# Kernel optimization log

Measured on AMD Instinct MI355X. Metric: run time of the kernel, lower is better.

The kernel has to match this reference:

```python
import jax, jax.numpy as jnp
import numpy as np


def _maxpool2(x):
    # 2x2 max pool, stride 2, valid padding (H, W even). x: [B,H,W,C]
    B, H, W, C = x.shape
    return x.reshape(B, H // 2, 2, W // 2, 2, C).max(axis=(2, 4))


def setup_inputs() -> dict:
    key = jax.random.key(0)
    ks = jax.random.split(key, 9)
    B, H, W, C = 8, 64, 64, 512
    cfg, ch = C // 8, C // 2
    std = 0.02
    return {
        "x": jax.random.normal(ks[0], (B, H, W, C), jnp.float32),
        "theta_w": jax.random.normal(ks[1], (C, cfg), jnp.float32) * std,
        "theta_b": jnp.zeros((cfg,), jnp.float32),
        "phi_w": jax.random.normal(ks[2], (C, cfg), jnp.float32) * std,
        "phi_b": jnp.zeros((cfg,), jnp.float32),
        "g_w": jax.random.normal(ks[3], (C, ch), jnp.float32) * std,
        "g_b": jnp.zeros((ch,), jnp.float32),
        "o3_w": jax.random.normal(ks[4], (ch, C), jnp.float32) * std,
        "o3_b": jnp.zeros((C,), jnp.float32),
        # original initializes gamma to 0; use 0.1 so the attention branch contributes
        "gamma": jnp.full((1,), 0.1, jnp.float32),
    }


def reference(x, theta_w, theta_b, phi_w, phi_b, g_w, g_b, o3_w, o3_b, gamma):
    B, H, W, C = x.shape
    cfg = theta_w.shape[1]
    ch = g_w.shape[1]
    hw = H * W
    hwd = (H // 2) * (W // 2)

    theta = jnp.einsum("bhwc,cf->bhwf", x, theta_w) + theta_b          # [B,H,W,cfg]
    phi = _maxpool2(jnp.einsum("bhwc,cf->bhwf", x, phi_w) + phi_b)     # [B,H/2,W/2,cfg]
    g = _maxpool2(jnp.einsum("bhwc,cg->bhwg", x, g_w) + g_b)           # [B,H/2,W/2,ch]

    theta_f = theta.reshape(B, hw, cfg)
    phi_f = phi.reshape(B, hwd, cfg)
    g_f = g.reshape(B, hwd, ch)

    # s[b,i,j] = phi[b,i] . theta[b,j]; softmax over j (last axis, Keras default)
    s = jnp.einsum("bif,bjf->bij", phi_f, theta_f)                     # [B,hwd,hw]
    beta = jax.nn.softmax(s, axis=-1)
    # o = matmul(beta, g, transpose_a=True): o[b,j,c] = sum_i beta[b,i,j] g[b,i,c]
    o = jnp.einsum("bij,bic->bjc", beta, g_f)                          # [B,hw,ch]
    o = o.reshape(B, H, W, ch)
    o = jnp.einsum("bhwg,gc->bhwc", o, o3_w) + o3_b                    # [B,H,W,C]
    return gamma * o + x
```

## Files before the change

kernel.cpp:

```cpp
#include <hip/hip_runtime.h>
#include <cstdint>

typedef short short8 __attribute__((ext_vector_type(8)));
typedef float floatx4 __attribute__((ext_vector_type(4)));

__device__ __forceinline__ unsigned short f2bf(float f) {
    unsigned int u = __builtin_bit_cast(unsigned int, f);
    u += 0x7FFFu + ((u >> 16) & 1u);
    return (unsigned short)(u >> 16);
}
__device__ __forceinline__ float bf2f(unsigned short h) {
    unsigned int u = ((unsigned int)h) << 16;
    return __builtin_bit_cast(float, u);
}

__device__ __forceinline__ void async_copy16(const void* g, void* lds) {
    __builtin_amdgcn_global_load_lds(
        (const __attribute__((address_space(1))) void*)g,
        (__attribute__((address_space(3))) void*)lds, 16, 0, 0);
}

__device__ __forceinline__ int swz(int row, int koff) {
    return koff ^ (((row >> 2) & 3) << 4);
}

template<bool AFP32, int EPI>
__global__ __launch_bounds__(256) void mfma_gemm(
    const void* __restrict__ Avoid, const unsigned short* __restrict__ B,
    void* __restrict__ Cout, const float* __restrict__ bias,
    const float* __restrict__ gamma, const float* __restrict__ resid,
    int lda, int ldb, int ldc, int K)
{
    __shared__ unsigned short As[4096];
    __shared__ unsigned short Bs[4096];

    const int tid = threadIdx.x;
    const int wv = tid >> 6, ln = tid & 63;
    const int r16 = ln & 15, q8 = ln >> 4;
    const int wm = (wv >> 1) * 64, wn = (wv & 1) * 64;
    const int m0 = blockIdx.y * 128, n0 = blockIdx.x * 128;

    floatx4 acc[4][4] = {};

    for (int k0 = 0; k0 < K; k0 += 32) {
        if (AFP32) {
            const float* Af = (const float*)Avoid;
            #pragma unroll
            for (int p = 0; p < 4; ++p) {
                int u = p * 256 + tid;
                int row = u >> 3, c4 = u & 7;
                float4 v = *(const float4*)(Af + (size_t)(m0 + row) * lda + k0 + c4 * 4);
                ushort4 h;
                h.x = f2bf(v.x); h.y = f2bf(v.y); h.z = f2bf(v.z); h.w = f2bf(v.w);
                *(ushort4*)&As[row * 32 + c4 * 4] = h;
            }
            #pragma unroll
            for (int q = 0; q < 2; ++q) {
                int chunk = wv * 2 + q;
                int e = (chunk << 9) + ln * 8;
                int row = e >> 5, col = e & 31;
                async_copy16(B + (size_t)(n0 + row) * ldb + (k0 + col), &Bs[chunk << 9]);
            }
        } else {
            const unsigned short* Ag = (const unsigned short*)Avoid;
            #pragma unroll
            for (int q = 0; q < 2; ++q) {
                int chunk = wv * 2 + q;
                int e = (chunk << 9) + ln * 8;
                int row = e >> 5, col = e & 31;
                async_copy16(Ag + (size_t)(m0 + row) * lda + (k0 + col), &As[chunk << 9]);
                async_copy16(B + (size_t)(n0 + row) * ldb + (k0 + col), &Bs[chunk << 9]);
            }
        }
        __syncthreads();

        short8 af[4], bff[4];
        #pragma unroll
        for (int i = 0; i < 4; ++i) {
            af[i]  = *(const short8*)&As[(wm + i * 16 + r16) * 32 + q8 * 8];
            bff[i] = *(const short8*)&Bs[(wn + i * 16 + r16) * 32 + q8 * 8];
        }
        #pragma unroll
        for (int mi = 0; mi < 4; ++mi)
            #pragma unroll
            for (int ni = 0; ni < 4; ++ni)
                acc[mi][ni] = __builtin_amdgcn_mfma_f32_16x16x32_bf16(
                    af[mi], bff[ni], acc[mi][ni], 0, 0, 0);
        __syncthreads();
    }

    if (EPI == 2) {
        float* C = (float*)Cout;
        const float gm = gamma[0];
        #pragma unroll
        for (int ni = 0; ni < 4; ++ni) {
            const int n = n0 + wn + ni * 16 + r16;
            const float bs = bias[n];
            #pragma unroll
            for (int mi = 0; mi < 4; ++mi)
                #pragma unroll
                for (int r = 0; r < 4; ++r) {
                    int m = m0 + wm + mi * 16 + q8 * 4 + r;
                    C[(size_t)m * ldc + n] = gm * (acc[mi][ni][r] + bs) + resid[(size_t)m * ldc + n];
                }
        }
    } else {
        unsigned short* C = (unsigned short*)Cout;
        #pragma unroll
        for (int ni = 0; ni < 4; ++ni) {
            const int n = n0 + wn + ni * 16 + r16;
            const float bs = bias[n];
            #pragma unroll
            for (int mi = 0; mi < 4; ++mi)
                #pragma unroll
                for (int r = 0; r < 4; ++r) {
                    int m = m0 + wm + mi * 16 + q8 * 4 + r;
                    C[(size_t)m * ldc + n] = f2bf(acc[mi][ni][r] + bs);
                }
        }
    }
}

__global__ __launch_bounds__(256) void phase1_l_kernel(
    const unsigned short* __restrict__ tpgF,
    const unsigned short* __restrict__ phiP,
    float* __restrict__ lbuf)
{
    __shared__ unsigned short th_s[8192];
    __shared__ unsigned short ph_s[4096];
    const int tid = threadIdx.x, wv = tid >> 6, ln = tid & 63;
    const int r16 = ln & 15, q8 = ln >> 4, lsub = ln >> 3, l8 = ln & 7;
    const int jsp = blockIdx.x, i0 = blockIdx.y * 64, b = blockIdx.z;

    #pragma unroll
    for (int q = 0; q < 2; ++q) {
        int chunk = wv * 2 + q, row = chunk * 8 + lsub;
        int so = swz(row, l8 * 8);
        async_copy16(phiP + (size_t)(b * 1024 + i0 + row) * 64 + so, &ph_s[chunk * 512]);
    }

    float colsum[4] = {0.f, 0.f, 0.f, 0.f};
    for (int jc = 0; jc < 8; ++jc) {
        const int j0 = jsp * 1024 + jc * 128;
        __syncthreads();
        #pragma unroll
        for (int q = 0; q < 4; ++q) {
            int chunk = wv * 4 + q, row = chunk * 8 + lsub;
            int so = swz(row, l8 * 8);
            async_copy16(tpgF + (size_t)(b * 4096 + j0 + row) * 384 + so, &th_s[chunk * 512]);
        }
        __syncthreads();

        floatx4 sacc[2][4] = {};
        #pragma unroll
        for (int ks = 0; ks < 2; ++ks) {
            short8 af[2], bf[4];
            #pragma unroll
            for (int mi = 0; mi < 2; ++mi)
                af[mi] = *(const short8*)&th_s[(wv * 32 + mi * 16 + r16) * 64 + swz(r16, ks * 32 + q8 * 8)];
            #pragma unroll
            for (int ni = 0; ni < 4; ++ni)
                bf[ni] = *(const short8*)&ph_s[(ni * 16 + r16) * 64 + swz(r16, ks * 32 + q8 * 8)];
            #pragma unroll
            for (int mi = 0; mi < 2; ++mi)
                #pragma unroll
                for (int ni = 0; ni < 4; ++ni)
                    sacc[mi][ni] = __builtin_amdgcn_mfma_f32_16x16x32_bf16(
                        af[mi], bf[ni], sacc[mi][ni], 0, 0, 0);
        }
        #pragma unroll
        for (int mi = 0; mi < 2; ++mi)
            #pragma unroll
            for (int ni = 0; ni < 4; ++ni)
                #pragma unroll
                for (int r = 0; r < 4; ++r)
                    colsum[ni] += __expf(sacc[mi][ni][r] - 20.f);
    }
    #pragma unroll
    for (int ni = 0; ni < 4; ++ni) {
        float s = colsum[ni];
        s += __shfl_xor(s, 16);
        s += __shfl_xor(s, 32);
        if (q8 == 0) atomicAdd(&lbuf[b * 1024 + i0 + ni * 16 + r16], s);
    }
}

__global__ __launch_bounds__(256) void attn_fused_kernel(
    const unsigned short* __restrict__ tpgF,
    const unsigned short* __restrict__ phiP,
    const unsigned short* __restrict__ gPT,
    unsigned short* __restrict__ o_)
{
    __shared__ unsigned short th_es[4096];
    __shared__ unsigned short ph_s[4096];
    __shared__ unsigned short gs[16384];

    const int tid = threadIdx.x, wv = tid >> 6, ln = tid & 63;
    const int r16 = ln & 15, q8 = ln >> 4, lsub = ln >> 3, l8 = ln & 7;
    const int j0 = blockIdx.x * 64, b = blockIdx.y;

    #pragma unroll
    for (int q = 0; q < 2; ++q) {
        int chunk = wv * 2 + q, row = chunk * 8 + lsub;
        int so = swz(row, l8 * 8);
        async_copy16(tpgF + (size_t)(b * 4096 + j0 + row) * 384 + so, &th_es[chunk * 512]);
    }
    __syncthreads();
    short8 thf[4][2];
    #pragma unroll
    for (int mi = 0; mi < 4; ++mi)
        #pragma unroll
        for (int ks = 0; ks < 2; ++ks)
            thf[mi][ks] = *(const short8*)&th_es[(mi * 16 + r16) * 64 + swz(r16, ks * 32 + q8 * 8)];

    floatx4 acc[4][4] = {};

    for (int i0 = 0; i0 < 1024; i0 += 64) {
        __syncthreads();
        #pragma unroll
        for (int q = 0; q < 2; ++q) {
            int chunk = wv * 2 + q, row = chunk * 8 + lsub;
            int so = swz(row, l8 * 8);
            async_copy16(phiP + (size_t)(b * 1024 + i0 + row) * 64 + so, &ph_s[chunk * 512]);
        }
        #pragma unroll
        for (int q = 0; q < 8; ++q) {
            int chunk = wv * 8 + q, c = chunk * 8 + lsub;
            int so = swz(c, l8 * 8);
            async_copy16(gPT + ((size_t)(b * 256 + c)) * 1024 + i0 + so, &gs[chunk * 512]);
        }
        __syncthreads();

        floatx4 sacc[4] = {};
        #pragma unroll
        for (int ks = 0; ks < 2; ++ks) {
            short8 pf = *(const short8*)&ph_s[(wv * 16 + r16) * 64 + swz(r16, ks * 32 + q8 * 8)];
            #pragma unroll
            for (int mi = 0; mi < 4; ++mi)
                sacc[mi] = __builtin_amdgcn_mfma_f32_16x16x32_bf16(
                    thf[mi][ks], pf, sacc[mi], 0, 0, 0);
        }
        #pragma unroll
        for (int mi = 0; mi < 4; ++mi)
            #pragma unroll
            for (int r = 0; r < 4; ++r) {
                int j = mi * 16 + q8 * 4 + r;
                th_es[j * 64 + (((wv ^ q8) << 4) | r16)] = f2bf(__expf(sacc[mi][r] - 20.f));
            }
        __syncthreads();

        #pragma unroll
        for (int ks = 0; ks < 2; ++ks) {
            short8 ef[4], gf[4];
            #pragma unroll
            for (int mi = 0; mi < 4; ++mi)
                ef[mi] = *(const short8*)&th_es[(mi * 16 + r16) * 64 + swz(r16, ks * 32 + q8 * 8)];
            #pragma unroll
            for (int ni = 0; ni < 4; ++ni)
                gf[ni] = *(const short8*)&gs[(wv * 64 + ni * 16 + r16) * 64 + swz(r16, ks * 32 + q8 * 8)];
            #pragma unroll
            for (int mi = 0; mi < 4; ++mi)
                #pragma unroll
                for (int ni = 0; ni < 4; ++ni)
                    acc[mi][ni] = __builtin_amdgcn_mfma_f32_16x16x32_bf16(
                        ef[mi], gf[ni], acc[mi][ni], 0, 0, 0);
        }
    }

    #pragma unroll
    for (int mi = 0; mi < 4; ++mi)
        #pragma unroll
        for (int ni = 0; ni < 4; ++ni)
            #pragma unroll
            for (int r = 0; r < 4; ++r) {
                int j = j0 + mi * 16 + q8 * 4 + r;
                int c = wv * 64 + ni * 16 + r16;
                o_[((size_t)b * 4096 + j) * 256 + c] = f2bf(acc[mi][ni][r]);
            }
}

__global__ __launch_bounds__(256) void prep_w_kernel(
    const float* __restrict__ theta_w, const float* __restrict__ phi_w,
    const float* __restrict__ g_w, const float* __restrict__ o3_w,
    const float* __restrict__ theta_b, const float* __restrict__ phi_b,
    const float* __restrict__ g_b,
    unsigned short* __restrict__ tpgwT, unsigned short* __restrict__ o3wT,
    float* __restrict__ biasTPG, float* __restrict__ lbuf)
{
    int t = blockIdx.x * 256 + threadIdx.x;
    if (t < 196608) {
        int n = t >> 9, k = t & 511;
        float v = (n < 64) ? theta_w[k * 64 + n]
                : (n < 128) ? phi_w[k * 64 + (n - 64)]
                : g_w[k * 256 + (n - 128)];
        tpgwT[t] = f2bf(v);
    } else if (t < 327680) {
        int e = t - 196608; int n = e >> 8, k = e & 255;
        o3wT[e] = f2bf(o3_w[k * 512 + n]);
    } else if (t < 328064) {
        int j = t - 327680;
        biasTPG[j] = (j < 64) ? theta_b[j] : (j < 128) ? phi_b[j - 64] : g_b[j - 128];
    } else if (t < 336256) {
        lbuf[t - 328064] = 0.f;
    }
}

__global__ __launch_bounds__(256) void maxpool_phi_kernel(
    const unsigned short* __restrict__ tpgF, unsigned short* __restrict__ phiP)
{
    int t = blockIdx.x * 256 + threadIdx.x;
    int f = t & 63, i = (t >> 6) & 1023, b = t >> 16;
    int ph = i >> 5, pw = i & 31;
    size_t base = ((size_t)(b * 64 + 2 * ph) * 64 + 2 * pw) * 384 + 64 + f;
    float v0 = bf2f(tpgF[base]),         v1 = bf2f(tpgF[base + 384]);
    float v2 = bf2f(tpgF[base + 24576]), v3 = bf2f(tpgF[base + 24576 + 384]);
    phiP[t] = f2bf(fmaxf(fmaxf(v0, v1), fmaxf(v2, v3)));
}

__global__ __launch_bounds__(256) void maxpoolT_g_kernel(
    const unsigned short* __restrict__ tpgF, const float* __restrict__ lbuf,
    unsigned short* __restrict__ gPT)
{
    __shared__ unsigned short tile[16][256];
    __shared__ float rls[16];
    int b = blockIdx.y, i0 = blockIdx.x * 16, c = threadIdx.x;
    if (c < 16) rls[c] = 1.0f / lbuf[b * 1024 + i0 + c];
    __syncthreads();
    #pragma unroll
    for (int il = 0; il < 16; ++il) {
        int i = i0 + il, ph = i >> 5, pw = i & 31;
        size_t base = ((size_t)(b * 64 + 2 * ph) * 64 + 2 * pw) * 384 + 128 + c;
        float v0 = bf2f(tpgF[base]),         v1 = bf2f(tpgF[base + 384]);
        float v2 = bf2f(tpgF[base + 24576]), v3 = bf2f(tpgF[base + 24576 + 384]);
        tile[il][c] = f2bf(fmaxf(fmaxf(v0, v1), fmaxf(v2, v3)) * rls[il]);
    }
    __syncthreads();
    unsigned short* dst = gPT + ((size_t)(b * 256 + c) * 1024 + i0);
    short8 v0, v1;
    #pragma unroll
    for (int il = 0; il < 8; ++il) { v0[il] = (short)tile[il][c]; v1[il] = (short)tile[il + 8][c]; }
    *(short8*)dst = v0;
    *(short8*)(dst + 8) = v1;
}

extern "C" void kernel_launch(void* const* d_in, const int* in_sizes, int n_in,
                              void* d_out, int out_size, void* d_ws, size_t ws_size,
                              hipStream_t stream)
{
    const float* x       = (const float*)d_in[0];
    const float* theta_w = (const float*)d_in[1];
    const float* theta_b = (const float*)d_in[2];
    const float* phi_w   = (const float*)d_in[3];
    const float* phi_b   = (const float*)d_in[4];
    const float* g_w     = (const float*)d_in[5];
    const float* g_b     = (const float*)d_in[6];
    const float* o3_w    = (const float*)d_in[7];
    const float* o3_b    = (const float*)d_in[8];
    const float* gamma   = (const float*)d_in[9];

    char* ws = (char*)d_ws;
    unsigned short* tpgwT  = (unsigned short*)(ws);
    unsigned short* o3wT   = (unsigned short*)(ws + 393216);
    float* biasTPG         = (float*)(ws + 655360);
    float* lbuf            = (float*)(ws + 656896);
    unsigned short* tpgF   = (unsigned short*)(ws + (1u << 20));
    unsigned short* phiP   = (unsigned short*)(ws + (1u << 20) + 25165824);
    unsigned short* gPT    = (unsigned short*)(ws + (1u << 20) + 26214400);
    unsigned short* o_     = (unsigned short*)(ws + (1u << 20) + 30408704);

    prep_w_kernel<<<1314, 256, 0, stream>>>(theta_w, phi_w, g_w, o3_w,
                                            theta_b, phi_b, g_b,
                                            tpgwT, o3wT, biasTPG, lbuf);
    mfma_gemm<true, 1><<<dim3(3, 256), 256, 0, stream>>>(
        x, tpgwT, tpgF, biasTPG, nullptr, nullptr, 512, 512, 384, 512);
    maxpool_phi_kernel<<<2048, 256, 0, stream>>>(tpgF, phiP);
    phase1_l_kernel<<<dim3(4, 16, 8), 256, 0, stream>>>(tpgF, phiP, lbuf);
    maxpoolT_g_kernel<<<dim3(64, 8), 256, 0, stream>>>(tpgF, lbuf, gPT);
    attn_fused_kernel<<<dim3(64, 8), 256, 0, stream>>>(tpgF, phiP, gPT, o_);
    mfma_gemm<false, 2><<<dim3(4, 256), 256, 0, stream>>>(
        o_, o3wT, d_out, o3_b, gamma, x, 256, 256, 512, 256);
}
```

Before: 236.0 us.

## Double-buffer phi/g tiles and widen attention block to 128 query rows

The fused attention kernel now runs 512-thread blocks covering 128 query rows, so each phi/g tile loaded into LDS is reused by two row halves. It also double-buffers the phi and g tiles, prefetching the next key tile with async LDS loads while computing the current one. Synchronisation uses explicit vmcnt/lgkmcnt waits and raw barriers. The cost is more LDS per block and half as many blocks in the grid, which may limit latency hiding.

Measured after the change: 233.1 us. About the same (-1.2%).

```diff
diff --git a/kernel.cpp b/kernel.cpp
--- a/kernel.cpp
+++ b/kernel.cpp
@@ -185,56 +185,81 @@
     }
 }
 
-__global__ __launch_bounds__(256) void attn_fused_kernel(
+__global__ __launch_bounds__(512) void attn_fused_kernel(
     const unsigned short* __restrict__ tpgF,
     const unsigned short* __restrict__ phiP,
     const unsigned short* __restrict__ gPT,
     unsigned short* __restrict__ o_)
 {
-    __shared__ unsigned short th_es[4096];
-    __shared__ unsigned short ph_s[4096];
-    __shared__ unsigned short gs[16384];
+    __shared__ unsigned short th_es[8192];
+    __shared__ unsigned short ph_s[2][4096];
+    __shared__ unsigned short gs[2][16384];
 
     const int tid = threadIdx.x, wv = tid >> 6, ln = tid & 63;
     const int r16 = ln & 15, q8 = ln >> 4, lsub = ln >> 3, l8 = ln & 7;
-    const int j0 = blockIdx.x * 64, b = blockIdx.y;
+    const int j0 = blockIdx.x * 128, b = blockIdx.y;
+    const int jh = wv >> 2, it = wv & 3;
 
     #pragma unroll
     for (int q = 0; q < 2; ++q) {
         int chunk = wv * 2 + q, row = chunk * 8 + lsub;
-        int so = swz(row, l8 * 8);
-        async_copy16(tpgF + (size_t)(b * 4096 + j0 + row) * 384 + so, &th_es[chunk * 512]);
-    }
-    __syncthreads();
+        async_copy16(tpgF + (size_t)(b * 4096 + j0 + row) * 384 + swz(row, l8 * 8),
+                     &th_es[chunk * 512]);
+    }
+    {
+        int row = wv * 8 + lsub;
+        async_copy16(phiP + (size_t)(b * 1024 + row) * 64 + swz(row, l8 * 8),
+                     &ph_s[0][wv * 512]);
+        #pragma unroll
+        for (int q = 0; q < 4; ++q) {
+            int chunk = wv * 4 + q, c = chunk * 8 + lsub;
+            async_copy16(gPT + (size_t)(b * 256 + c) * 1024 + swz(c, l8 * 8),
+                         &gs[0][chunk * 512]);
+        }
+    }
+    asm volatile("s_waitcnt vmcnt(5)" ::: "memory");
+    __builtin_amdgcn_sched_barrier(0);
+    __builtin_amdgcn_s_barrier();
+    __builtin_amdgcn_sched_barrier(0);
+
     short8 thf[4][2];
     #pragma unroll
     for (int mi = 0; mi < 4; ++mi)
         #pragma unroll
         for (int ks = 0; ks < 2; ++ks)
-            thf[mi][ks] = *(const short8*)&th_es[(mi * 16 + r16) * 64 + swz(r16, ks * 32 + q8 * 8)];
+            thf[mi][ks] = *(const short8*)&th_es[(jh * 64 + mi * 16 + r16) * 64
+                                                 + swz(r16, ks * 32 + q8 * 8)];
+    asm volatile("s_waitcnt lgkmcnt(0)" ::: "memory");
+    __builtin_amdgcn_sched_barrier(0);
 
     floatx4 acc[4][4] = {};
 
-    for (int i0 = 0; i0 < 1024; i0 += 64) {
-        __syncthreads();
-        #pragma unroll
-        for (int q = 0; q < 2; ++q) {
-            int chunk = wv * 2 + q, row = chunk * 8 + lsub;
-            int so = swz(row, l8 * 8);
-            async_copy16(phiP + (size_t)(b * 1024 + i0 + row) * 64 + so, &ph_s[chunk * 512]);
-        }
-        #pragma unroll
-        for (int q = 0; q < 8; ++q) {
-            int chunk = wv * 8 + q, c = chunk * 8 + lsub;
-            int so = swz(c, l8 * 8);
-            async_copy16(gPT + ((size_t)(b * 256 + c)) * 1024 + i0 + so, &gs[chunk * 512]);
-        }
-        __syncthreads();
+    for (int t = 0; t < 16; ++t) {
+        const int buf = t & 1, nbuf = buf ^ 1;
+        if (t < 15) {
+            const int i0n = (t + 1) * 64;
+            int row = wv * 8 + lsub;
+            async_copy16(phiP + (size_t)(b * 1024 + i0n + row) * 64 + swz(row, l8 * 8),
+                         &ph_s[nbuf][wv * 512]);
+            #pragma unroll
+            for (int q = 0; q < 4; ++q) {
+                int chunk = wv * 4 + q, c = chunk * 8 + lsub;
+                async_copy16(gPT + (size_t)(b * 256 + c) * 1024 + i0n + swz(c, l8 * 8),
+                             &gs[nbuf][chunk * 512]);
+            }
+            asm volatile("s_waitcnt vmcnt(5)" ::: "memory");
+        } else {
+            asm volatile("s_waitcnt vmcnt(0)" ::: "memory");
+        }
+        __builtin_amdgcn_sched_barrier(0);
+        __builtin_amdgcn_s_barrier();
+        __builtin_amdgcn_sched_barrier(0);
 
         floatx4 sacc[4] = {};
         #pragma unroll
         for (int ks = 0; ks < 2; ++ks) {
-            short8 pf = *(const short8*)&ph_s[(wv * 16 + r16) * 64 + swz(r16, ks * 32 + q8 * 8)];
+            short8 pf = *(const short8*)&ph_s[buf][(it * 16 + r16) * 64
+                                                   + swz(r16, ks * 32 + q8 * 8)];
             #pragma unroll
             for (int mi = 0; mi < 4; ++mi)
                 sacc[mi] = __builtin_amdgcn_mfma_f32_16x16x32_bf16(
@@ -244,20 +269,25 @@
         for (int mi = 0; mi < 4; ++mi)
             #pragma unroll
             for (int r = 0; r < 4; ++r) {
-                int j = mi * 16 + q8 * 4 + r;
-                th_es[j * 64 + (((wv ^ q8) << 4) | r16)] = f2bf(__expf(sacc[mi][r] - 20.f));
-            }
-        __syncthreads();
+                int j = jh * 64 + mi * 16 + q8 * 4 + r;
+                th_es[j * 64 + (((it ^ q8) << 4) | r16)] = f2bf(__expf(sacc[mi][r] - 20.f));
+            }
+        asm volatile("s_waitcnt lgkmcnt(0)" ::: "memory");
+        __builtin_amdgcn_sched_barrier(0);
+        __builtin_amdgcn_s_barrier();
+        __builtin_amdgcn_sched_barrier(0);
 
         #pragma unroll
         for (int ks = 0; ks < 2; ++ks) {
             short8 ef[4], gf[4];
             #pragma unroll
             for (int mi = 0; mi < 4; ++mi)
-                ef[mi] = *(const short8*)&th_es[(mi * 16 + r16) * 64 + swz(r16, ks * 32 + q8 * 8)];
+                ef[mi] = *(const short8*)&th_es[(jh * 64 + mi * 16 + r16) * 64
+                                                + swz(r16, ks * 32 + q8 * 8)];
             #pragma unroll
             for (int ni = 0; ni < 4; ++ni)
-                gf[ni] = *(const short8*)&gs[(wv * 64 + ni * 16 + r16) * 64 + swz(r16, ks * 32 + q8 * 8)];
+                gf[ni] = *(const short8*)&gs[buf][(it * 64 + ni * 16 + r16) * 64
+                                                  + swz(r16, ks * 32 + q8 * 8)];
             #pragma unroll
             for (int mi = 0; mi < 4; ++mi)
                 #pragma unroll
@@ -265,6 +295,10 @@
                     acc[mi][ni] = __builtin_amdgcn_mfma_f32_16x16x32_bf16(
                         ef[mi], gf[ni], acc[mi][ni], 0, 0, 0);
         }
+        asm volatile("s_waitcnt lgkmcnt(0)" ::: "memory");
+        __builtin_amdgcn_sched_barrier(0);
+        __builtin_amdgcn_s_barrier();
+        __builtin_amdgcn_sched_barrier(0);
     }
 
     #pragma unroll
@@ -273,8 +307,8 @@
         for (int ni = 0; ni < 4; ++ni)
             #pragma unroll
             for (int r = 0; r < 4; ++r) {
-                int j = j0 + mi * 16 + q8 * 4 + r;
-                int c = wv * 64 + ni * 16 + r16;
+                int j = j0 + jh * 64 + mi * 16 + q8 * 4 + r;
+                int c = it * 64 + ni * 16 + r16;
                 o_[((size_t)b * 4096 + j) * 256 + c] = f2bf(acc[mi][ni][r]);
             }
 }
@@ -376,7 +410,7 @@
     maxpool_phi_kernel<<<2048, 256, 0, stream>>>(tpgF, phiP);
     phase1_l_kernel<<<dim3(4, 16, 8), 256, 0, stream>>>(tpgF, phiP, lbuf);
     maxpoolT_g_kernel<<<dim3(64, 8), 256, 0, stream>>>(tpgF, lbuf, gPT);
-    attn_fused_kernel<<<dim3(64, 8), 256, 0, stream>>>(tpgF, phiP, gPT, o_);
+    attn_fused_kernel<<<dim3(32, 8), 512, 0, stream>>>(tpgF, phiP, gPT, o_);
     mfma_gemm<false, 2><<<dim3(4, 256), 256, 0, stream>>>(
         o_, o3wT, d_out, o3_b, gamma, x, 256, 256, 512, 256);
 }
```

## Double GEMM K-tile to 64 with XOR-swizzled LDS layout

Applied to the files above, without the earlier changes.

Raises the K step of the MFMA GEMM from 32 to 64, so each tile load is followed by two MFMA sub-steps and the number of barrier pairs per K is halved. The LDS layout for both A and B is XOR-swizzled per row (column chunk index ^ row&7), applied on the async global-to-LDS copies and the fp32→bf16 store path, to avoid bank conflicts on the short8 fragment reads. LDS use per block doubles, which may lower occupancy.

Result: slower. 241.1 us (+2.2%).

```diff
diff --git a/kernel.cpp b/kernel.cpp
--- a/kernel.cpp
+++ b/kernel.cpp
@@ -22,6 +22,9 @@
 
 __device__ __forceinline__ int swz(int row, int koff) {
     return koff ^ (((row >> 2) & 3) << 4);
+}
+__device__ __forceinline__ int swzK(int row, int koff) {
+    return koff ^ ((row & 7) << 3);
 }
 
 template<bool AFP32, int EPI>
@@ -31,61 +34,63 @@
     const float* __restrict__ gamma, const float* __restrict__ resid,
     int lda, int ldb, int ldc, int K)
 {
-    __shared__ unsigned short As[4096];
-    __shared__ unsigned short Bs[4096];
+    __shared__ unsigned short As[8192];
+    __shared__ unsigned short Bs[8192];
 
     const int tid = threadIdx.x;
     const int wv = tid >> 6, ln = tid & 63;
-    const int r16 = ln & 15, q8 = ln >> 4;
+    const int r16 = ln & 15, q8 = ln >> 4, lsub = ln >> 3, l8 = ln & 7;
     const int wm = (wv >> 1) * 64, wn = (wv & 1) * 64;
     const int m0 = blockIdx.y * 128, n0 = blockIdx.x * 128;
 
     floatx4 acc[4][4] = {};
 
-    for (int k0 = 0; k0 < K; k0 += 32) {
+    for (int k0 = 0; k0 < K; k0 += 64) {
         if (AFP32) {
             const float* Af = (const float*)Avoid;
             #pragma unroll
-            for (int p = 0; p < 4; ++p) {
+            for (int p = 0; p < 8; ++p) {
                 int u = p * 256 + tid;
-                int row = u >> 3, c4 = u & 7;
+                int row = u >> 4, c4 = u & 15;
                 float4 v = *(const float4*)(Af + (size_t)(m0 + row) * lda + k0 + c4 * 4);
                 ushort4 h;
                 h.x = f2bf(v.x); h.y = f2bf(v.y); h.z = f2bf(v.z); h.w = f2bf(v.w);
-                *(ushort4*)&As[row * 32 + c4 * 4] = h;
-            }
-            #pragma unroll
-            for (int q = 0; q < 2; ++q) {
-                int chunk = wv * 2 + q;
-                int e = (chunk << 9) + ln * 8;
-                int row = e >> 5, col = e & 31;
-                async_copy16(B + (size_t)(n0 + row) * ldb + (k0 + col), &Bs[chunk << 9]);
+                *(ushort4*)&As[row * 64 + ((c4 * 4) ^ ((row & 7) << 3))] = h;
             }
         } else {
             const unsigned short* Ag = (const unsigned short*)Avoid;
             #pragma unroll
-            for (int q = 0; q < 2; ++q) {
-                int chunk = wv * 2 + q;
-                int e = (chunk << 9) + ln * 8;
-                int row = e >> 5, col = e & 31;
-                async_copy16(Ag + (size_t)(m0 + row) * lda + (k0 + col), &As[chunk << 9]);
-                async_copy16(B + (size_t)(n0 + row) * ldb + (k0 + col), &Bs[chunk << 9]);
-            }
-        }
-        __syncthreads();
-
-        short8 af[4], bff[4];
-        #pragma unroll
-        for (int i = 0; i < 4; ++i) {
-            af[i]  = *(const short8*)&As[(wm + i * 16 + r16) * 32 + q8 * 8];
-            bff[i] = *(const short8*)&Bs[(wn + i * 16 + r16) * 32 + q8 * 8];
-        }
-        #pragma unroll
-        for (int mi = 0; mi < 4; ++mi)
-            #pragma unroll
-            for (int ni = 0; ni < 4; ++ni)
-                acc[mi][ni] = __builtin_amdgcn_mfma_f32_16x16x32_bf16(
-                    af[mi], bff[ni], acc[mi][ni], 0, 0, 0);
+            for (int q = 0; q < 4; ++q) {
+                int chunk = wv * 4 + q, row = chunk * 8 + lsub;
+                async_copy16(Ag + (size_t)(m0 + row) * lda + k0 + ((l8 ^ (row & 7)) * 8),
+                             &As[chunk * 512]);
+            }
+        }
+        #pragma unroll
+        for (int q = 0; q < 4; ++q) {
+            int chunk = wv * 4 + q, row = chunk * 8 + lsub;
+            async_copy16(B + (size_t)(n0 + row) * ldb + k0 + ((l8 ^ (row & 7)) * 8),
+                         &Bs[chunk * 512]);
+        }
+        __syncthreads();
+
+        #pragma unroll
+        for (int ks = 0; ks < 2; ++ks) {
+            short8 af[4], bff[4];
+            #pragma unroll
+            for (int i = 0; i < 4; ++i) {
+                int ra = wm + i * 16 + r16;
+                af[i]  = *(const short8*)&As[ra * 64 + swzK(ra, ks * 32 + q8 * 8)];
+                int rb = wn + i * 16 + r16;
+                bff[i] = *(const short8*)&Bs[rb * 64 + swzK(rb, ks * 32 + q8 * 8)];
+            }
+            #pragma unroll
+            for (int mi = 0; mi < 4; ++mi)
+                #pragma unroll
+                for (int ni = 0; ni < 4; ++ni)
+                    acc[mi][ni] = __builtin_amdgcn_mfma_f32_16x16x32_bf16(
+                        af[mi], bff[ni], acc[mi][ni], 0, 0, 0);
+        }
         __syncthreads();
     }
 
```

## Fuse 2x2 maxpool of phi and g into projection GEMM epilogue

Applied to the files above, without the earlier changes.

The projection GEMM epilogue now stages bf16 outputs in shared memory and performs the 2x2 max pooling directly, writing pooled phi and transposed pooled g. Only theta is written to global memory, compacted to a 64-wide row. This removes the two standalone maxpool kernels and most of the 384-wide intermediate traffic. Because g is now produced before the softmax denominators exist, the 1/l normalization moves into the attention kernel, which scales the exponentials by a per-row reciprocal. In exchange the epilogue gains extra shared memory and block-wide synchronizations.

Result: no change. 240.3 us (+1.8%).

```diff
diff --git a/kernel.cpp b/kernel.cpp
--- a/kernel.cpp
+++ b/kernel.cpp
@@ -29,10 +29,12 @@
     const void* __restrict__ Avoid, const unsigned short* __restrict__ B,
     void* __restrict__ Cout, const float* __restrict__ bias,
     const float* __restrict__ gamma, const float* __restrict__ resid,
+    unsigned short* __restrict__ phiP, unsigned short* __restrict__ gPT,
     int lda, int ldb, int ldc, int K)
 {
     __shared__ unsigned short As[4096];
     __shared__ unsigned short Bs[4096];
+    __shared__ unsigned short pool_s[(EPI == 3) ? 8192 : 8];
 
     const int tid = threadIdx.x;
     const int wv = tid >> 6, ln = tid & 63;
@@ -105,18 +107,71 @@
                 }
         }
     } else {
-        unsigned short* C = (unsigned short*)Cout;
+        const int bx = blockIdx.x, by = blockIdx.y;
+        unsigned short hv[4][4][4];
         #pragma unroll
         for (int ni = 0; ni < 4; ++ni) {
-            const int n = n0 + wn + ni * 16 + r16;
-            const float bs = bias[n];
+            const float bs = bias[n0 + wn + ni * 16 + r16];
             #pragma unroll
             for (int mi = 0; mi < 4; ++mi)
                 #pragma unroll
-                for (int r = 0; r < 4; ++r) {
-                    int m = m0 + wm + mi * 16 + q8 * 4 + r;
-                    C[(size_t)m * ldc + n] = f2bf(acc[mi][ni][r] + bs);
+                for (int r = 0; r < 4; ++r)
+                    hv[ni][mi][r] = f2bf(acc[mi][ni][r] + bs);
+        }
+        if (bx == 0 && wn == 0) {
+            unsigned short* C = (unsigned short*)Cout;
+            #pragma unroll
+            for (int ni = 0; ni < 4; ++ni)
+                #pragma unroll
+                for (int mi = 0; mi < 4; ++mi)
+                    #pragma unroll
+                    for (int r = 0; r < 4; ++r) {
+                        int m = m0 + wm + mi * 16 + q8 * 4 + r;
+                        C[(size_t)m * 64 + ni * 16 + r16] = hv[ni][mi][r];
+                    }
+        }
+        const int bpool = by >> 5, ip0 = (by & 31) * 32;
+        for (int hf = (bx == 0) ? 1 : 0; hf < 2; ++hf) {
+            if (wn == hf * 64) {
+                #pragma unroll
+                for (int ni = 0; ni < 4; ++ni)
+                    #pragma unroll
+                    for (int mi = 0; mi < 4; ++mi)
+                        #pragma unroll
+                        for (int r = 0; r < 4; ++r)
+                            pool_s[(wm + mi * 16 + q8 * 4 + r) * 64 + ni * 16 + r16]
+                                = hv[ni][mi][r];
+            }
+            __syncthreads();
+            if (bx == 0) {
+                int i = tid >> 3, c0 = (tid & 7) * 8;
+                short8 out;
+                #pragma unroll
+                for (int cc = 0; cc < 8; ++cc) {
+                    int c = c0 + cc;
+                    float v0 = bf2f(pool_s[(2 * i) * 64 + c]);
+                    float v1 = bf2f(pool_s[(2 * i + 1) * 64 + c]);
+                    float v2 = bf2f(pool_s[(64 + 2 * i) * 64 + c]);
+                    float v3 = bf2f(pool_s[(65 + 2 * i) * 64 + c]);
+                    out[cc] = (short)f2bf(fmaxf(fmaxf(v0, v1), fmaxf(v2, v3)));
                 }
+                *(short8*)&phiP[((size_t)(bpool * 1024 + ip0 + i)) * 64 + c0] = out;
+            } else {
+                int c = tid >> 2, ib = (tid & 3) * 8;
+                short8 out;
+                #pragma unroll
+                for (int ii = 0; ii < 8; ++ii) {
+                    int i = ib + ii;
+                    float v0 = bf2f(pool_s[(2 * i) * 64 + c]);
+                    float v1 = bf2f(pool_s[(2 * i + 1) * 64 + c]);
+                    float v2 = bf2f(pool_s[(64 + 2 * i) * 64 + c]);
+                    float v3 = bf2f(pool_s[(65 + 2 * i) * 64 + c]);
+                    out[ii] = (short)f2bf(fmaxf(fmaxf(v0, v1), fmaxf(v2, v3)));
+                }
+                int cg = (bx - 1) * 128 + hf * 64 + c;
+                *(short8*)&gPT[((size_t)(bpool * 256 + cg)) * 1024 + ip0 + ib] = out;
+            }
+            __syncthreads();
         }
     }
 }
@@ -147,7 +202,7 @@
         for (int q = 0; q < 4; ++q) {
             int chunk = wv * 4 + q, row = chunk * 8 + lsub;
             int so = swz(row, l8 * 8);
-            async_copy16(tpgF + (size_t)(b * 4096 + j0 + row) * 384 + so, &th_s[chunk * 512]);
+            async_copy16(tpgF + (size_t)(b * 4096 + j0 + row) * 64 + so, &th_s[chunk * 512]);
         }
         __syncthreads();
 
@@ -189,6 +244,7 @@
     const unsigned short* __restrict__ tpgF,
     const unsigned short* __restrict__ phiP,
     const unsigned short* __restrict__ gPT,
+    const float* __restrict__ lbuf,
     unsigned short* __restrict__ o_)
 {
     __shared__ unsigned short th_es[4096];
@@ -203,7 +259,7 @@
     for (int q = 0; q < 2; ++q) {
         int chunk = wv * 2 + q, row = chunk * 8 + lsub;
         int so = swz(row, l8 * 8);
-        async_copy16(tpgF + (size_t)(b * 4096 + j0 + row) * 384 + so, &th_es[chunk * 512]);
+        async_copy16(tpgF + (size_t)(b * 4096 + j0 + row) * 64 + so, &th_es[chunk * 512]);
     }
     __syncthreads();
     short8 thf[4][2];
@@ -217,6 +273,7 @@
 
     for (int i0 = 0; i0 < 1024; i0 += 64) {
         __syncthreads();
+        float lv = lbuf[b * 1024 + i0 + wv * 16 + r16];
         #pragma unroll
         for (int q = 0; q < 2; ++q) {
             int chunk = wv * 2 + q, row = chunk * 8 + lsub;
@@ -240,12 +297,14 @@
                 sacc[mi] = __builtin_amdgcn_mfma_f32_16x16x32_bf16(
                     thf[mi][ks], pf, sacc[mi], 0, 0, 0);
         }
+        const float rl = 1.0f / lv;
         #pragma unroll
         for (int mi = 0; mi < 4; ++mi)
             #pragma unroll
             for (int r = 0; r < 4; ++r) {
                 int j = mi * 16 + q8 * 4 + r;
-                th_es[j * 64 + (((wv ^ q8) << 4) | r16)] = f2bf(__expf(sacc[mi][r] - 20.f));
+                th_es[j * 64 + (((wv ^ q8) << 4) | r16)] =
+                    f2bf(__expf(sacc[mi][r] - 20.f) * rl);
             }
         __syncthreads();
 
@@ -305,44 +364,6 @@
     }
 }
 
-__global__ __launch_bounds__(256) void maxpool_phi_kernel(
-    const unsigned short* __restrict__ tpgF, unsigned short* __restrict__ phiP)
-{
-    int t = blockIdx.x * 256 + threadIdx.x;
-    int f = t & 63, i = (t >> 6) & 1023, b = t >> 16;
-    int ph = i >> 5, pw = i & 31;
-    size_t base = ((size_t)(b * 64 + 2 * ph) * 64 + 2 * pw) * 384 + 64 + f;
-    float v0 = bf2f(tpgF[base]),         v1 = bf2f(tpgF[base + 384]);
-    float v2 = bf2f(tpgF[base + 24576]), v3 = bf2f(tpgF[base + 24576 + 384]);
-    phiP[t] = f2bf(fmaxf(fmaxf(v0, v1), fmaxf(v2, v3)));
-}
-
-__global__ __launch_bounds__(256) void maxpoolT_g_kernel(
-    const unsigned short* __restrict__ tpgF, const float* __restrict__ lbuf,
-    unsigned short* __restrict__ gPT)
-{
-    __shared__ unsigned short tile[16][256];
-    __shared__ float rls[16];
-    int b = blockIdx.y, i0 = blockIdx.x * 16, c = threadIdx.x;
-    if (c < 16) rls[c] = 1.0f / lbuf[b * 1024 + i0 + c];
-    __syncthreads();
-    #pragma unroll
-    for (int il = 0; il < 16; ++il) {
-        int i = i0 + il, ph = i >> 5, pw = i & 31;
-        size_t base = ((size_t)(b * 64 + 2 * ph) * 64 + 2 * pw) * 384 + 128 + c;
-        float v0 = bf2f(tpgF[base]),         v1 = bf2f(tpgF[base + 384]);
-        float v2 = bf2f(tpgF[base + 24576]), v3 = bf2f(tpgF[base + 24576 + 384]);
-        tile[il][c] = f2bf(fmaxf(fmaxf(v0, v1), fmaxf(v2, v3)) * rls[il]);
-    }
-    __syncthreads();
-    unsigned short* dst = gPT + ((size_t)(b * 256 + c) * 1024 + i0);
-    short8 v0, v1;
-    #pragma unroll
-    for (int il = 0; il < 8; ++il) { v0[il] = (short)tile[il][c]; v1[il] = (short)tile[il + 8][c]; }
-    *(short8*)dst = v0;
-    *(short8*)(dst + 8) = v1;
-}
-
 extern "C" void kernel_launch(void* const* d_in, const int* in_sizes, int n_in,
                               void* d_out, int out_size, void* d_ws, size_t ws_size,
                               hipStream_t stream)
@@ -371,12 +392,10 @@
     prep_w_kernel<<<1314, 256, 0, stream>>>(theta_w, phi_w, g_w, o3_w,
                                             theta_b, phi_b, g_b,
                                             tpgwT, o3wT, biasTPG, lbuf);
-    mfma_gemm<true, 1><<<dim3(3, 256), 256, 0, stream>>>(
-        x, tpgwT, tpgF, biasTPG, nullptr, nullptr, 512, 512, 384, 512);
-    maxpool_phi_kernel<<<2048, 256, 0, stream>>>(tpgF, phiP);
+    mfma_gemm<true, 3><<<dim3(3, 256), 256, 0, stream>>>(
+        x, tpgwT, tpgF, biasTPG, nullptr, nullptr, phiP, gPT, 512, 512, 64, 512);
     phase1_l_kernel<<<dim3(4, 16, 8), 256, 0, stream>>>(tpgF, phiP, lbuf);
-    maxpoolT_g_kernel<<<dim3(64, 8), 256, 0, stream>>>(tpgF, lbuf, gPT);
-    attn_fused_kernel<<<dim3(64, 8), 256, 0, stream>>>(tpgF, phiP, gPT, o_);
+    attn_fused_kernel<<<dim3(64, 8), 256, 0, stream>>>(tpgF, phiP, gPT, lbuf, o_);
     mfma_gemm<false, 2><<<dim3(4, 256), 256, 0, stream>>>(
-        o_, o3wT, d_out, o3_b, gamma, x, 256, 256, 512, 256);
-}
+        o_, o3wT, d_out, o3_b, gamma, x, nullptr, nullptr, 256, 256, 512, 256);
+}
```
